# Kernel optimization log

Hardware: AMD Instinct MI355X
Metric: run time of the kernel (lower is better)

Reference implementation:

```python
import jax, jax.numpy as jnp
import numpy as np

B, Q, HIST, HID, NH, D, BS, NBLK, NUMB = 8, 512, 1536, 4096, 32, 128, 64, 32, 256


def _rope(x, pos):
    # GPT-NeoX-style rotary used by Falcon: rotate_half over full head_dim.
    Dh = x.shape[-1]
    inv = 1.0 / (10000.0 ** (jnp.arange(0, Dh, 2, dtype=jnp.float32) / Dh))  # [D/2]
    ang = pos.astype(jnp.float32)[:, None] * inv[None, :]                    # [T, D/2]
    cos = jnp.concatenate([jnp.cos(ang), jnp.cos(ang)], -1)[None, :, None, :]
    sin = jnp.concatenate([jnp.sin(ang), jnp.sin(ang)], -1)[None, :, None, :]
    half = Dh // 2
    rot = jnp.concatenate([-x[..., half:], x[..., :half]], -1)
    return x * cos + rot * sin


def setup_inputs() -> dict:
    key = jax.random.key(0)
    ks = jax.random.split(key, 6)
    hidden_states = jax.random.normal(ks[0], (1, B * Q, HID), jnp.float32) * 0.02
    qkv_weight = jax.random.normal(ks[1], ((NH + 2) * D, HID), jnp.float32) * 0.02
    dense_weight = jax.random.normal(ks[2], (HID, NH * D), jnp.float32) * 0.02
    past_key = jax.random.normal(ks[3], (NUMB, BS, 1, D), jnp.float32) * 0.02
    past_value = jax.random.normal(ks[4], (NUMB, BS, 1, D), jnp.float32) * 0.02
    q_start_loc = (jnp.arange(B) * Q).astype(jnp.int32)
    q_seq_length = jnp.full((B,), Q, jnp.int32)
    history_lengths = jnp.full((B,), HIST, jnp.int32)
    # each sequence owns NBLK distinct cache blocks (shuffled block table)
    block_offsets = jax.random.permutation(ks[5], NUMB).reshape(B, NBLK).astype(jnp.int32)
    position_ids_1d = (history_lengths[:, None] + jnp.arange(Q, dtype=jnp.int32)[None, :]).reshape(-1)
    return dict(hidden_states=hidden_states, qkv_weight=qkv_weight, dense_weight=dense_weight,
                past_key=past_key, past_value=past_value, q_start_loc=q_start_loc,
                q_seq_length=q_seq_length, history_lengths=history_lengths,
                block_offsets=block_offsets, position_ids_1d=position_ids_1d)


def reference(hidden_states, qkv_weight, dense_weight, past_key, past_value,
              q_start_loc, q_seq_length, history_lengths, block_offsets, position_ids_1d):
    T = hidden_states.shape[1]
    Bn = block_offsets.shape[0]
    Qn = T // Bn
    Dh = past_key.shape[-1]
    BSz = past_key.shape[1]
    # fused QKV projection
    fused = hidden_states @ qkv_weight.T                      # [1, T, (NH+2)*D]
    NHh = fused.shape[-1] // Dh - 2
    qkv = fused.reshape(1, T, NHh + 2, Dh)
    q = qkv[:, :, :NHh]                                       # [1, T, NH, D]
    k = qkv[:, :, NHh:NHh + 1]                                 # [1, T, 1, D]
    v = qkv[:, :, NHh + 1:]                                    # [1, T, 1, D]
    # inline rotary embedding on q, k
    q = _rope(q, position_ids_1d)
    k = _rope(k, position_ids_1d)
    # fill_kv_cache: scatter new K/V into paged cache via block table
    seq_id = jnp.repeat(jnp.arange(Bn), Qn)                   # [T]
    pos = position_ids_1d.astype(jnp.int32)                   # absolute kv position
    blk = block_offsets[seq_id, pos // BSz]                   # [T] physical block id
    off = pos % BSz
    past_key = past_key.at[blk, off].set(k.reshape(T, 1, Dh))
    past_value = past_value.at[blk, off].set(v.reshape(T, 1, Dh))
    # paged_attention_fwd: gather per-sequence K/V from paged cache
    KVc = block_offsets.shape[1] * BSz                        # kv capacity == kv_len here
    kseq = past_key[block_offsets].reshape(Bn, KVc, Dh)       # [B, KV, D] (1 kv head squeezed)
    vseq = past_value[block_offsets].reshape(Bn, KVc, Dh)
    qb = q.reshape(Bn, Qn, NHh, Dh)
    scale = 1.0 / jnp.sqrt(jnp.float32(Dh))
    scores = jnp.einsum('bqhd,bkd->bhqk', qb, kseq) * scale   # [B, H, Q, KV]
    qpos = history_lengths[:, None] + jnp.arange(Qn)[None, :] # [B, Q]
    mask = jnp.arange(KVc)[None, None, :] <= qpos[:, :, None] # causal + length mask
    scores = jnp.where(mask[:, None, :, :], scores, jnp.float32(-1e30))
    attn = jax.nn.softmax(scores, axis=-1)
    out = jnp.einsum('bhqk,bkd->bqhd', attn, vseq)            # [B, Q, H, D]
    out = out.reshape(1, T, NHh * Dh)
    return out @ dense_weight.T                                # [1, T, hidden]
```

## Files before the change

### kernel.cpp

```cpp
#include <hip/hip_runtime.h>

typedef __attribute__((ext_vector_type(8))) short bf16x8;
typedef __attribute__((ext_vector_type(4))) float f32x4;
typedef __attribute__((ext_vector_type(16))) float f32x16;
typedef __attribute__((ext_vector_type(2))) unsigned int u32x2;

constexpr int B_ = 8, Q_ = 512, HIST_ = 1536, HID_ = 4096, NH_ = 32, D_ = 128;
constexpr int BS_ = 64, NBLK_ = 32;
constexpr int T_ = B_ * Q_;
constexpr int QKVN = (NH_ + 2) * D_;
constexpr int KVC = NBLK_ * BS_;

__device__ __forceinline__ unsigned short f2bf(float f) {
  union { float f; unsigned u; } v; v.f = f;
  unsigned r = v.u + 0x7FFFu + ((v.u >> 16) & 1u);
  return (unsigned short)(r >> 16);
}
__device__ __forceinline__ float bf2f(unsigned short s) {
  union { unsigned u; float f; } v; v.u = ((unsigned)s) << 16;
  return v.f;
}
__device__ __forceinline__ int cvtpk_bf16(float lo, float hi) {
  int r;
  asm("v_cvt_pk_bf16_f32 %0, %1, %2" : "=v"(r) : "v"(lo), "v"(hi));
  return r;
}

__global__ void k_conv(const float* __restrict__ in, unsigned short* __restrict__ out, int n4) {
  int i = blockIdx.x * blockDim.x + threadIdx.x;
  int stride = gridDim.x * blockDim.x;
  for (; i < n4; i += stride) {
    float4 v = reinterpret_cast<const float4*>(in)[i];
    ushort4 o;
    o.x = f2bf(v.x); o.y = f2bf(v.y); o.z = f2bf(v.z); o.w = f2bf(v.w);
    reinterpret_cast<ushort4*>(out)[i] = o;
  }
}

__global__ void k_gemm_bt(const unsigned short* __restrict__ A,
                          const unsigned short* __restrict__ Bm,
                          float* __restrict__ Cf, unsigned short* __restrict__ Cb,
                          int M, int N, int K, int ldc) {
  __shared__ alignas(16) unsigned short lA[128 * 64];
  __shared__ alignas(16) unsigned short lB[128 * 64];
  const int tid = threadIdx.x;
  const int lane = tid & 63;
  const int w = tid >> 6;
  const int wr = w >> 1, wc = w & 1;
  const int n0 = blockIdx.x * 128, m0 = blockIdx.y * 128;
  const int lr = lane & 15, lk = lane >> 4;
  const int srow = lane >> 3;
  const int scol = (lane & 7) * 8;

  f32x4 acc[4][4];
#pragma unroll
  for (int m = 0; m < 4; ++m)
#pragma unroll
    for (int n = 0; n < 4; ++n) acc[m][n] = f32x4{0.f, 0.f, 0.f, 0.f};

  for (int k0 = 0; k0 < K; k0 += 64) {
#pragma unroll
    for (int i = 0; i < 4; ++i) {
      int seg = w * 4 + i;
      const unsigned short* ga = A + (size_t)(m0 + seg * 8 + srow) * K + k0 + scol;
      const unsigned short* gb = Bm + (size_t)(n0 + seg * 8 + srow) * K + k0 + scol;
      __builtin_amdgcn_global_load_lds((const __attribute__((address_space(1))) void*)ga,
                                       (__attribute__((address_space(3))) void*)(&lA[seg * 512]), 16, 0, 0);
      __builtin_amdgcn_global_load_lds((const __attribute__((address_space(1))) void*)gb,
                                       (__attribute__((address_space(3))) void*)(&lB[seg * 512]), 16, 0, 0);
    }
    __syncthreads();
#pragma unroll
    for (int kk = 0; kk < 2; ++kk) {
      bf16x8 af[4], bfr[4];
      const int sl = (kk * 4 + lk) * 8;
#pragma unroll
      for (int m = 0; m < 4; ++m)
        af[m] = *reinterpret_cast<bf16x8*>(&lA[(wr * 64 + m * 16 + lr) * 64 + sl]);
#pragma unroll
      for (int n = 0; n < 4; ++n)
        bfr[n] = *reinterpret_cast<bf16x8*>(&lB[(wc * 64 + n * 16 + lr) * 64 + sl]);
#pragma unroll
      for (int m = 0; m < 4; ++m)
#pragma unroll
        for (int n = 0; n < 4; ++n)
          acc[m][n] = __builtin_amdgcn_mfma_f32_16x16x32_bf16(af[m], bfr[n], acc[m][n], 0, 0, 0);
    }
    __syncthreads();
  }
#pragma unroll
  for (int m = 0; m < 4; ++m)
#pragma unroll
    for (int n = 0; n < 4; ++n)
#pragma unroll
      for (int j = 0; j < 4; ++j) {
        int r = m0 + wr * 64 + m * 16 + lk * 4 + j;
        int c = n0 + wc * 64 + n * 16 + lr;
        if (Cb) Cb[(size_t)r * ldc + c] = f2bf(acc[m][n][j]);
        else Cf[(size_t)r * ldc + c] = acc[m][n][j];
      }
}

__global__ void k_rope(const unsigned short* __restrict__ fused,
                       const int* __restrict__ pos_ids,
                       unsigned short* __restrict__ qb,
                       unsigned short* __restrict__ kseq,
                       unsigned short* __restrict__ vtg) {
  int t = blockIdx.x;
  int d = threadIdx.x;
  int b = t >> 9, q = t & 511;
  int pos = pos_ids[t];
  __shared__ float cs[64], sn[64];
  if (d < 64) {
    float inv = powf(10000.f, -(float)d * (1.f / 64.f));
    float ang = (float)pos * inv;
    cs[d] = cosf(ang);
    sn[d] = sinf(ang);
  }
  __syncthreads();
  const float scale = 0.1275174313836907f;
  float c = cs[d & 63], s = sn[d & 63];
  const unsigned short* row = fused + (size_t)t * QKVN;
#pragma unroll 4
  for (int h = 0; h < NH_; ++h) {
    float x = bf2f(row[h * D_ + d]);
    float xr = (d < 64) ? -bf2f(row[h * D_ + d + 64]) : bf2f(row[h * D_ + d - 64]);
    qb[(((size_t)(b * NH_ + h)) * Q_ + q) * D_ + d] = f2bf((x * c + xr * s) * scale);
  }
  {
    float x = bf2f(row[NH_ * D_ + d]);
    float xr = (d < 64) ? -bf2f(row[NH_ * D_ + d + 64]) : bf2f(row[NH_ * D_ + d - 64]);
    kseq[((size_t)b * KVC + pos) * D_ + d] = f2bf(x * c + xr * s);
  }
  vtg[((size_t)b * D_ + d) * KVC + pos] = row[(NH_ + 1) * D_ + d];
}

__global__ void k_gather(const float* __restrict__ pk, const float* __restrict__ pv,
                         const int* __restrict__ bo,
                         unsigned short* __restrict__ kseq, unsigned short* __restrict__ vtg) {
  __shared__ unsigned short vl[64 * 140];
  const int ptile = blockIdx.x;
  const int b = ptile / (HIST_ / 64);
  const int p0 = (ptile % (HIST_ / 64)) * 64;
  const int tid = threadIdx.x;
  const int blk = bo[b * NBLK_ + (p0 >> 6)];
#pragma unroll
  for (int c = 0; c < 8; ++c) {
    int u = c * 256 + tid;
    int p = u >> 5, d4 = u & 31;
    size_t src = ((size_t)blk * BS_ + p) * D_ + d4 * 4;
    float4 kv = *reinterpret_cast<const float4*>(pk + src);
    ushort4 ko;
    ko.x = f2bf(kv.x); ko.y = f2bf(kv.y); ko.z = f2bf(kv.z); ko.w = f2bf(kv.w);
    *reinterpret_cast<ushort4*>(kseq + ((size_t)b * KVC + p0 + p) * D_ + d4 * 4) = ko;
    float4 vv = *reinterpret_cast<const float4*>(pv + src);
    ushort4 vo;
    vo.x = f2bf(vv.x); vo.y = f2bf(vv.y); vo.z = f2bf(vv.z); vo.w = f2bf(vv.w);
    *reinterpret_cast<ushort4*>(&vl[p * 140 + d4 * 4]) = vo;
  }
  __syncthreads();
#pragma unroll
  for (int c = 0; c < 4; ++c) {
    int u = c * 256 + tid;
    int d = u >> 3, pg = u & 7;
    bf16x8 vv8;
#pragma unroll
    for (int i = 0; i < 8; ++i) vv8[i] = (short)vl[(pg * 8 + i) * 140 + d];
    *reinterpret_cast<bf16x8*>(vtg + ((size_t)b * D_ + d) * KVC + p0 + pg * 8) = vv8;
  }
}

__global__ __launch_bounds__(512, 2) void k_attn(const unsigned short* __restrict__ qb,
                       const unsigned short* __restrict__ kseq,
                       const unsigned short* __restrict__ vtg,
                       const int* __restrict__ histL,
                       unsigned short* __restrict__ outb) {
  __shared__ alignas(16) unsigned short kl[2][64 * 128];
  __shared__ alignas(16) unsigned short vt[2][128 * 64];
  const int qt = blockIdx.x, hp = blockIdx.y, b = blockIdx.z;
  const int tid = threadIdx.x, lane = tid & 63, w = tid >> 6;
  const int H = lane >> 5, q = lane & 31;
  const int h = hp * 8 + w;
  const int q0 = qt * 32;
  const int hist = histL[b];
  const unsigned short* kseq_b = kseq + (size_t)b * KVC * D_;
  const unsigned short* vtg_b  = vtg + (size_t)b * D_ * KVC;

  const unsigned short* qrow = qb + (((size_t)(b * NH_ + h)) * Q_ + q0 + q) * D_;
  bf16x8 aq[8];
#pragma unroll
  for (int ds = 0; ds < 8; ++ds)
    aq[ds] = *reinterpret_cast<const bf16x8*>(qrow + ds * 16 + H * 8);

  f32x16 o[4];
#pragma unroll
  for (int db = 0; db < 4; ++db)
#pragma unroll
    for (int r = 0; r < 16; ++r) o[db][r] = 0.f;
  float m = -1e30f, l = 0.f;

  const int ntiles = (hist + q0 + 32 + 63) >> 6;

  auto STAGE = [&](int bufi, int kv0) {
#pragma unroll
    for (int c = 0; c < 2; ++c) {
      int ob = c * 8192 + tid * 16;
      int row = ob >> 8;
      int sp = (ob >> 4) & 15;
      const unsigned short* src = kseq_b + (size_t)(kv0 + row) * D_ + (((sp ^ (row & 15)) << 3));
      __builtin_amdgcn_global_load_lds((const __attribute__((address_space(1))) void*)src,
          (__attribute__((address_space(3))) void*)(&kl[bufi][c * 4096 + w * 512]), 16, 0, 0);
    }
#pragma unroll
    for (int c = 0; c < 2; ++c) {
      int ob = c * 8192 + tid * 16;
      int row = ob >> 7;
      int sp = (ob >> 4) & 7;
      const unsigned short* src = vtg_b + (size_t)row * KVC + kv0 + (((sp ^ (row & 7)) << 3));
      __builtin_amdgcn_global_load_lds((const __attribute__((address_space(1))) void*)src,
          (__attribute__((address_space(3))) void*)(&vt[bufi][c * 4096 + w * 512]), 16, 0, 0);
    }
  };

  STAGE(0, 0);
  __syncthreads();

  for (int it = 0; it < ntiles; ++it) {
    const int cur = it & 1;
    if (it + 1 < ntiles) STAGE(cur ^ 1, (it + 1) * 64);
    const unsigned short* kb = kl[cur];
    const unsigned short* vb = vt[cur];

    f32x16 sa = f32x16{0.f,0.f,0.f,0.f,0.f,0.f,0.f,0.f,0.f,0.f,0.f,0.f,0.f,0.f,0.f,0.f};
    f32x16 sb = sa, sc = sa, sd = sa;
#pragma unroll
    for (int ds = 0; ds < 4; ++ds) {
      const int sl = ((2 * ds + H) ^ (q & 15)) << 3;
      bf16x8 k0 = *reinterpret_cast<const bf16x8*>(kb + q * 128 + sl);
      bf16x8 k1 = *reinterpret_cast<const bf16x8*>(kb + (32 + q) * 128 + sl);
      sa = __builtin_amdgcn_mfma_f32_32x32x16_bf16(k0, aq[ds], sa, 0, 0, 0);
      sc = __builtin_amdgcn_mfma_f32_32x32x16_bf16(k1, aq[ds], sc, 0, 0, 0);
    }
#pragma unroll
    for (int ds = 4; ds < 8; ++ds) {
      const int sl = ((2 * ds + H) ^ (q & 15)) << 3;
      bf16x8 k0 = *reinterpret_cast<const bf16x8*>(kb + q * 128 + sl);
      bf16x8 k1 = *reinterpret_cast<const bf16x8*>(kb + (32 + q) * 128 + sl);
      sb = __builtin_amdgcn_mfma_f32_32x32x16_bf16(k0, aq[ds], sb, 0, 0, 0);
      sd = __builtin_amdgcn_mfma_f32_32x32x16_bf16(k1, aq[ds], sd, 0, 0, 0);
    }
    f32x16 s0 = sa + sb;
    f32x16 s1 = sc + sd;

    if (it == ntiles - 1) {
      const int limit = hist + q0 + q - it * 64 - 4 * H;
#pragma unroll
      for (int r = 0; r < 16; ++r) {
        const int koff = (r & 3) + 8 * ((r >> 2) & 1) + 16 * (r >> 3);
        if (koff > limit) s0[r] = -1e30f;
        if (32 + koff > limit) s1[r] = -1e30f;
      }
    }

    float pmax = s0[0];
#pragma unroll
    for (int r = 1; r < 16; ++r) pmax = fmaxf(pmax, s0[r]);
#pragma unroll
    for (int r = 0; r < 16; ++r) pmax = fmaxf(pmax, s1[r]);
    pmax = fmaxf(pmax, __shfl_xor(pmax, 32));
    if (__any(pmax > m + 11.54f)) {
      float mn = fmaxf(m, pmax);
      float al = exp2f(m - mn);
      m = mn;
      l *= al;
#pragma unroll
      for (int db = 0; db < 4; ++db)
#pragma unroll
        for (int r = 0; r < 16; ++r) o[db][r] *= al;
    }
    float rs = 0.f;
#pragma unroll
    for (int r = 0; r < 16; ++r) { s0[r] = exp2f(s0[r] - m); rs += s0[r]; }
#pragma unroll
    for (int r = 0; r < 16; ++r) { s1[r] = exp2f(s1[r] - m); rs += s1[r]; }
    rs += __shfl_xor(rs, 32);
    l += rs;

#pragma unroll
    for (int s = 0; s < 4; ++s) {
      float p0, p1, p2, p3, p4, p5, p6, p7;
      if (s == 0)      { p0=s0[0];p1=s0[1];p2=s0[2];p3=s0[3];p4=s0[4];p5=s0[5];p6=s0[6];p7=s0[7]; }
      else if (s == 1) { p0=s0[8];p1=s0[9];p2=s0[10];p3=s0[11];p4=s0[12];p5=s0[13];p6=s0[14];p7=s0[15]; }
      else if (s == 2) { p0=s1[0];p1=s1[1];p2=s1[2];p3=s1[3];p4=s1[4];p5=s1[5];p6=s1[6];p7=s1[7]; }
      else             { p0=s1[8];p1=s1[9];p2=s1[10];p3=s1[11];p4=s1[12];p5=s1[13];p6=s1[14];p7=s1[15]; }
      int c01 = cvtpk_bf16(p0, p1);
      int c23 = cvtpk_bf16(p2, p3);
      int c45 = cvtpk_bf16(p4, p5);
      int c67 = cvtpk_bf16(p6, p7);
      u32x2 rA = __builtin_amdgcn_permlane32_swap(c01, c45, false, false);
      u32x2 rB = __builtin_amdgcn_permlane32_swap(c23, c67, false, false);
      union { unsigned wds[4]; bf16x8 v; } uu;
      uu.wds[0] = rA[0]; uu.wds[1] = rB[0]; uu.wds[2] = rA[1]; uu.wds[3] = rB[1];
#pragma unroll
      for (int db = 0; db < 4; ++db) {
        const int row = db * 32 + q;
        bf16x8 vf = *reinterpret_cast<const bf16x8*>(vb + row * 64 + ((((2 * s + H) ^ (row & 7))) << 3));
        o[db] = __builtin_amdgcn_mfma_f32_32x32x16_bf16(vf, uu.v, o[db], 0, 0, 0);
      }
    }
    __syncthreads();
  }

  const float il = 1.f / l;
  unsigned short* orow = outb + (size_t)(b * Q_ + q0 + q) * (NH_ * D_) + h * D_;
#pragma unroll
  for (int db = 0; db < 4; ++db)
#pragma unroll
    for (int rr = 0; rr < 4; ++rr) {
      ushort4 st;
      st.x = f2bf(o[db][rr * 4 + 0] * il);
      st.y = f2bf(o[db][rr * 4 + 1] * il);
      st.z = f2bf(o[db][rr * 4 + 2] * il);
      st.w = f2bf(o[db][rr * 4 + 3] * il);
      *reinterpret_cast<ushort4*>(orow + db * 32 + rr * 8 + 4 * H) = st;
    }
}

extern "C" void kernel_launch(void* const* d_in, const int* in_sizes, int n_in,
                              void* d_out, int out_size, void* d_ws, size_t ws_size,
                              hipStream_t stream) {
  const float* hidden = (const float*)d_in[0];
  const float* qkvw   = (const float*)d_in[1];
  const float* densew = (const float*)d_in[2];
  const float* pk     = (const float*)d_in[3];
  const float* pv     = (const float*)d_in[4];
  const int* histL    = (const int*)d_in[7];
  const int* bo       = (const int*)d_in[8];
  const int* posids   = (const int*)d_in[9];
  float* out = (float*)d_out;

  char* ws = (char*)d_ws;
  unsigned short* ws_hidden = (unsigned short*)(ws);
  unsigned short* ws_w      = (unsigned short*)(ws + 33554432);
  unsigned short* ws_fused  = (unsigned short*)(ws + 69206016);
  unsigned short* ws_q      = (unsigned short*)(ws + 104857600);
  unsigned short* ws_k      = (unsigned short*)(ws + 138412032);
  unsigned short* ws_vt     = (unsigned short*)(ws + 142606336);
  unsigned short* ws_attn   = ws_hidden;

  k_conv<<<2048, 256, 0, stream>>>(hidden, ws_hidden, T_ * HID_ / 4);
  k_conv<<<2048, 256, 0, stream>>>(qkvw, ws_w, QKVN * HID_ / 4);
  dim3 g1(QKVN / 128, T_ / 128);
  k_gemm_bt<<<g1, 256, 0, stream>>>(ws_hidden, ws_w, nullptr, ws_fused, T_, QKVN, HID_, QKVN);
  k_rope<<<T_, 128, 0, stream>>>(ws_fused, posids, ws_q, ws_k, ws_vt);
  k_gather<<<B_ * (HIST_ / 64), 256, 0, stream>>>(pk, pv, bo, ws_k, ws_vt);
  dim3 ga(Q_ / 32, NH_ / 8, B_);
  k_attn<<<ga, 512, 0, stream>>>(ws_q, ws_k, ws_vt, histL, ws_attn);
  k_conv<<<2048, 256, 0, stream>>>(densew, ws_w, HID_ * HID_ / 4);
  dim3 g2(HID_ / 128, T_ / 128);
  k_gemm_bt<<<g2, 256, 0, stream>>>(ws_attn, ws_w, out, nullptr, T_, HID_, HID_, HID_);
}
```

Baseline: 600.8 us.

## Replace GEMM with 256x256 double-buffered, swizzled, XCD-remapped pipelined kernel

```diff
diff --git a/kernel.cpp b/kernel.cpp
--- a/kernel.cpp
+++ b/kernel.cpp
@@ -37,67 +37,109 @@
   }
 }
 
-__global__ void k_gemm_bt(const unsigned short* __restrict__ A,
+__global__ __launch_bounds__(512, 2) void k_gemm256(const unsigned short* __restrict__ A,
                           const unsigned short* __restrict__ Bm,
                           float* __restrict__ Cf, unsigned short* __restrict__ Cb,
-                          int M, int N, int K, int ldc) {
-  __shared__ alignas(16) unsigned short lA[128 * 64];
-  __shared__ alignas(16) unsigned short lB[128 * 64];
-  const int tid = threadIdx.x;
-  const int lane = tid & 63;
-  const int w = tid >> 6;
-  const int wr = w >> 1, wc = w & 1;
-  const int n0 = blockIdx.x * 128, m0 = blockIdx.y * 128;
+                          int MB, int K, int ldc) {
+  extern __shared__ unsigned short smem[];
+  unsigned short* sA = smem;
+  unsigned short* sB = smem + 32768;
+  const int tid = threadIdx.x, lane = tid & 63, w = tid >> 6;
+  const int wr = w >> 2, wc = w & 3;
   const int lr = lane & 15, lk = lane >> 4;
-  const int srow = lane >> 3;
-  const int scol = (lane & 7) * 8;
-
-  f32x4 acc[4][4];
-#pragma unroll
-  for (int m = 0; m < 4; ++m)
-#pragma unroll
-    for (int n = 0; n < 4; ++n) acc[m][n] = f32x4{0.f, 0.f, 0.f, 0.f};
-
-  for (int k0 = 0; k0 < K; k0 += 64) {
-#pragma unroll
-    for (int i = 0; i < 4; ++i) {
-      int seg = w * 4 + i;
-      const unsigned short* ga = A + (size_t)(m0 + seg * 8 + srow) * K + k0 + scol;
-      const unsigned short* gb = Bm + (size_t)(n0 + seg * 8 + srow) * K + k0 + scol;
-      __builtin_amdgcn_global_load_lds((const __attribute__((address_space(1))) void*)ga,
-                                       (__attribute__((address_space(3))) void*)(&lA[seg * 512]), 16, 0, 0);
-      __builtin_amdgcn_global_load_lds((const __attribute__((address_space(1))) void*)gb,
-                                       (__attribute__((address_space(3))) void*)(&lB[seg * 512]), 16, 0, 0);
-    }
-    __syncthreads();
-#pragma unroll
-    for (int kk = 0; kk < 2; ++kk) {
-      bf16x8 af[4], bfr[4];
-      const int sl = (kk * 4 + lk) * 8;
-#pragma unroll
-      for (int m = 0; m < 4; ++m)
-        af[m] = *reinterpret_cast<bf16x8*>(&lA[(wr * 64 + m * 16 + lr) * 64 + sl]);
-#pragma unroll
-      for (int n = 0; n < 4; ++n)
-        bfr[n] = *reinterpret_cast<bf16x8*>(&lB[(wc * 64 + n * 16 + lr) * 64 + sl]);
-#pragma unroll
-      for (int m = 0; m < 4; ++m)
+
+  const int nwg = gridDim.x, orig = blockIdx.x;
+  const int q8 = nwg >> 3, r8 = nwg & 7, xcd = orig & 7;
+  const int wg = (xcd < r8 ? xcd * (q8 + 1) : r8 * (q8 + 1) + (xcd - r8) * q8) + (orig >> 3);
+  const int m0 = (wg % MB) * 256;
+  const int n0 = (wg / MB) * 256;
+  const int NT = K >> 6;
+
+  f32x4 acc[8][4];
+#pragma unroll
+  for (int mf = 0; mf < 8; ++mf)
+#pragma unroll
+    for (int nf = 0; nf < 4; ++nf) acc[mf][nf] = f32x4{0.f, 0.f, 0.f, 0.f};
+
+  auto stage = [&](const unsigned short* __restrict__ Mat, int rbase, unsigned short* regionBase,
+                   int ts, int half) {
+    const int di = ts < NT ? ts : NT - 1;
+    const size_t k0 = (size_t)di << 6;
+    char* hb = (char*)(regionBase + (ts & 1) * 16384 + half * 8192);
+#pragma unroll
+    for (int c = 0; c < 2; ++c) {
+      const int ob = c * 8192 + (w << 10) + (lane << 4);
+      const int row = ob >> 7;
+      const int sl = ((ob >> 4) & 7) ^ (row & 7);
+      const unsigned short* src = Mat + (size_t)(rbase + half * 128 + row) * K + k0 + sl * 8;
+      __builtin_amdgcn_global_load_lds((const __attribute__((address_space(1))) void*)src,
+          (__attribute__((address_space(3))) void*)(hb + c * 8192 + (w << 10)), 16, 0, 0);
+    }
+  };
+
+  stage(A, m0, sA, 0, 0); stage(A, m0, sA, 0, 1);
+  stage(Bm, n0, sB, 0, 0); stage(Bm, n0, sB, 0, 1);
+  stage(Bm, n0, sB, 1, 0); stage(Bm, n0, sB, 1, 1);
+  asm volatile("s_waitcnt vmcnt(4)" ::: "memory");
+  __builtin_amdgcn_s_barrier();
+
+  for (int t = 0; t < NT; ++t) {
+    const int cur = t & 1;
+    unsigned short* a_t = sA + cur * 16384 + wr * 8192;
+    unsigned short* b_t = sB + cur * 16384 + (wc >> 1) * 8192;
+    bf16x8 bfr[4][2];
+#pragma unroll
+    for (int p = 0; p < 4; ++p) {
+      bf16x8 af[2][2];
+#pragma unroll
+      for (int m = 0; m < 2; ++m)
+#pragma unroll
+        for (int kk = 0; kk < 2; ++kk) {
+          const int r = p * 32 + m * 16 + lr;
+          af[m][kk] = *reinterpret_cast<bf16x8*>(&a_t[r * 64 + ((((kk << 2) + lk) ^ (r & 7)) << 3)]);
+        }
+      if (p == 0) {
 #pragma unroll
         for (int n = 0; n < 4; ++n)
-          acc[m][n] = __builtin_amdgcn_mfma_f32_16x16x32_bf16(af[m], bfr[n], acc[m][n], 0, 0, 0);
-    }
-    __syncthreads();
-  }
-#pragma unroll
-  for (int m = 0; m < 4; ++m)
-#pragma unroll
-    for (int n = 0; n < 4; ++n)
+#pragma unroll
+          for (int kk = 0; kk < 2; ++kk) {
+            const int rb = (wc & 1) * 64 + n * 16 + lr;
+            bfr[n][kk] = *reinterpret_cast<bf16x8*>(&b_t[rb * 64 + ((((kk << 2) + lk) ^ (rb & 7)) << 3)]);
+          }
+      }
+      if (p == 0) stage(A, m0, sA, t + 1, 0);
+      if (p == 1) { stage(A, m0, sA, t + 1, 1); stage(Bm, n0, sB, t + 2, 0); }
+      if (p == 2) stage(Bm, n0, sB, t + 2, 1);
+      asm volatile("" ::: "memory");
+      __builtin_amdgcn_s_barrier();
+      asm volatile("s_waitcnt lgkmcnt(0)" ::: "memory");
+      __builtin_amdgcn_sched_barrier(0);
+      __builtin_amdgcn_s_setprio(1);
+#pragma unroll
+      for (int m = 0; m < 2; ++m)
+#pragma unroll
+        for (int n = 0; n < 4; ++n)
+#pragma unroll
+          for (int kk = 0; kk < 2; ++kk)
+            acc[p * 2 + m][n] = __builtin_amdgcn_mfma_f32_16x16x32_bf16(af[m][kk], bfr[n][kk], acc[p * 2 + m][n], 0, 0, 0);
+      __builtin_amdgcn_s_setprio(0);
+      if (p == 3) asm volatile("s_waitcnt vmcnt(4)" ::: "memory");
+      asm volatile("" ::: "memory");
+      __builtin_amdgcn_s_barrier();
+    }
+  }
+  asm volatile("s_waitcnt vmcnt(0)" ::: "memory");
+
+#pragma unroll
+  for (int mf = 0; mf < 8; ++mf)
+#pragma unroll
+    for (int nf = 0; nf < 4; ++nf)
 #pragma unroll
       for (int j = 0; j < 4; ++j) {
-        int r = m0 + wr * 64 + m * 16 + lk * 4 + j;
-        int c = n0 + wc * 64 + n * 16 + lr;
-        if (Cb) Cb[(size_t)r * ldc + c] = f2bf(acc[m][n][j]);
-        else Cf[(size_t)r * ldc + c] = acc[m][n][j];
+        const int rr = m0 + wr * 128 + mf * 16 + lk * 4 + j;
+        const int cc = n0 + wc * 64 + nf * 16 + lr;
+        if (Cb) Cb[(size_t)rr * ldc + cc] = f2bf(acc[mf][nf][j]);
+        else Cf[(size_t)rr * ldc + cc] = acc[mf][nf][j];
       }
 }
 
@@ -350,13 +392,13 @@
 
   k_conv<<<2048, 256, 0, stream>>>(hidden, ws_hidden, T_ * HID_ / 4);
   k_conv<<<2048, 256, 0, stream>>>(qkvw, ws_w, QKVN * HID_ / 4);
-  dim3 g1(QKVN / 128, T_ / 128);
-  k_gemm_bt<<<g1, 256, 0, stream>>>(ws_hidden, ws_w, nullptr, ws_fused, T_, QKVN, HID_, QKVN);
+  k_gemm256<<<dim3((T_ / 256) * (QKVN / 256)), 512, 131072, stream>>>(
+      ws_hidden, ws_w, nullptr, ws_fused, T_ / 256, HID_, QKVN);
   k_rope<<<T_, 128, 0, stream>>>(ws_fused, posids, ws_q, ws_k, ws_vt);
   k_gather<<<B_ * (HIST_ / 64), 256, 0, stream>>>(pk, pv, bo, ws_k, ws_vt);
   dim3 ga(Q_ / 32, NH_ / 8, B_);
   k_attn<<<ga, 512, 0, stream>>>(ws_q, ws_k, ws_vt, histL, ws_attn);
   k_conv<<<2048, 256, 0, stream>>>(densew, ws_w, HID_ * HID_ / 4);
-  dim3 g2(HID_ / 128, T_ / 128);
-  k_gemm_bt<<<g2, 256, 0, stream>>>(ws_attn, ws_w, out, nullptr, T_, HID_, HID_, HID_);
-}
+  k_gemm256<<<dim3((T_ / 256) * (HID_ / 256)), 512, 131072, stream>>>(
+      ws_attn, ws_w, out, nullptr, T_ / 256, HID_, HID_);
+}
```

New measurement: 580.7 us. 1.03x faster.

## Rewrite GEMM with 128x256 tiles, triple-buffered LDS pipeline and swizzle

Applied to the files above, without the earlier changes.

```diff
diff --git a/kernel.cpp b/kernel.cpp
--- a/kernel.cpp
+++ b/kernel.cpp
@@ -37,20 +37,25 @@
   }
 }
 
-__global__ void k_gemm_bt(const unsigned short* __restrict__ A,
+#define SW_(r) ((((r) & 3)) ^ (((r) >> 2) & 3))
+
+__global__ __launch_bounds__(512, 4) void k_gemm(const unsigned short* __restrict__ A,
                           const unsigned short* __restrict__ Bm,
                           float* __restrict__ Cf, unsigned short* __restrict__ Cb,
-                          int M, int N, int K, int ldc) {
-  __shared__ alignas(16) unsigned short lA[128 * 64];
-  __shared__ alignas(16) unsigned short lB[128 * 64];
-  const int tid = threadIdx.x;
-  const int lane = tid & 63;
-  const int w = tid >> 6;
-  const int wr = w >> 1, wc = w & 1;
-  const int n0 = blockIdx.x * 128, m0 = blockIdx.y * 128;
+                          int MB, int K, int ldc) {
+  extern __shared__ unsigned short smem[];
+  unsigned short* sA = smem;
+  unsigned short* sB = smem + 12288;
+  const int tid = threadIdx.x, lane = tid & 63, w = tid >> 6;
+  const int wr = w >> 2, wc = w & 3;
   const int lr = lane & 15, lk = lane >> 4;
-  const int srow = lane >> 3;
-  const int scol = (lane & 7) * 8;
+
+  const int nwg = gridDim.x, orig = blockIdx.x;
+  const int q8 = nwg >> 3, r8 = nwg & 7, xcd = orig & 7;
+  const int wg = (xcd < r8 ? xcd * (q8 + 1) : r8 * (q8 + 1) + (xcd - r8) * q8) + (orig >> 3);
+  const int m0 = (wg % MB) * 128;
+  const int n0 = (wg / MB) * 256;
+  const int NT = K >> 5;
 
   f32x4 acc[4][4];
 #pragma unroll
@@ -58,46 +63,77 @@
 #pragma unroll
     for (int n = 0; n < 4; ++n) acc[m][n] = f32x4{0.f, 0.f, 0.f, 0.f};
 
-  for (int k0 = 0; k0 < K; k0 += 64) {
-#pragma unroll
-    for (int i = 0; i < 4; ++i) {
-      int seg = w * 4 + i;
-      const unsigned short* ga = A + (size_t)(m0 + seg * 8 + srow) * K + k0 + scol;
-      const unsigned short* gb = Bm + (size_t)(n0 + seg * 8 + srow) * K + k0 + scol;
-      __builtin_amdgcn_global_load_lds((const __attribute__((address_space(1))) void*)ga,
-                                       (__attribute__((address_space(3))) void*)(&lA[seg * 512]), 16, 0, 0);
-      __builtin_amdgcn_global_load_lds((const __attribute__((address_space(1))) void*)gb,
-                                       (__attribute__((address_space(3))) void*)(&lB[seg * 512]), 16, 0, 0);
-    }
-    __syncthreads();
-#pragma unroll
-    for (int kk = 0; kk < 2; ++kk) {
-      bf16x8 af[4], bfr[4];
-      const int sl = (kk * 4 + lk) * 8;
-#pragma unroll
-      for (int m = 0; m < 4; ++m)
-        af[m] = *reinterpret_cast<bf16x8*>(&lA[(wr * 64 + m * 16 + lr) * 64 + sl]);
+  auto stage = [&](int bi, int k0) {
+    {
+      const int ob = tid << 4;
+      const int row = ob >> 6;
+      const int s = (ob >> 4) & 3;
+      const unsigned short* src = A + (size_t)(m0 + row) * K + k0 + ((s ^ SW_(row)) << 3);
+      __builtin_amdgcn_global_load_lds((const __attribute__((address_space(1))) void*)src,
+          (__attribute__((address_space(3))) void*)((char*)sA + bi * 8192 + (tid << 4)), 16, 0, 0);
+    }
+#pragma unroll
+    for (int c = 0; c < 2; ++c) {
+      const int u = (c << 9) + tid;
+      const int ob = u << 4;
+      const int row = ob >> 6;
+      const int s = (ob >> 4) & 3;
+      const unsigned short* src = Bm + (size_t)(n0 + row) * K + k0 + ((s ^ SW_(row)) << 3);
+      __builtin_amdgcn_global_load_lds((const __attribute__((address_space(1))) void*)src,
+          (__attribute__((address_space(3))) void*)((char*)sB + bi * 16384 + (ob)), 16, 0, 0);
+    }
+  };
+
+  stage(0, 0);
+  stage(1, NT > 1 ? 32 : 0);
+  asm volatile("s_waitcnt vmcnt(3)" ::: "memory");
+  __builtin_amdgcn_s_barrier();
+  asm volatile("" ::: "memory");
+
+  int cur = 0;
+  for (int t = 0; t < NT; ++t) {
+    int sb = cur + 2; if (sb > 2) sb -= 3;
+    const int ts = (t + 2 < NT) ? (t + 2) : (NT - 1);
+    stage(sb, ts << 5);
+
+    const unsigned short* a_t = sA + cur * 4096;
+    const unsigned short* b_t = sB + cur * 8192;
+    bf16x8 af[4], bfr[4];
+#pragma unroll
+    for (int m = 0; m < 4; ++m) {
+      const int r = wr * 64 + m * 16 + lr;
+      af[m] = *reinterpret_cast<const bf16x8*>(&a_t[r * 32 + ((lk ^ SW_(r)) << 3)]);
+    }
+#pragma unroll
+    for (int n = 0; n < 4; ++n) {
+      const int r = wc * 64 + n * 16 + lr;
+      bfr[n] = *reinterpret_cast<const bf16x8*>(&b_t[r * 32 + ((lk ^ SW_(r)) << 3)]);
+    }
+    __builtin_amdgcn_s_setprio(1);
+#pragma unroll
+    for (int m = 0; m < 4; ++m)
 #pragma unroll
       for (int n = 0; n < 4; ++n)
-        bfr[n] = *reinterpret_cast<bf16x8*>(&lB[(wc * 64 + n * 16 + lr) * 64 + sl]);
-#pragma unroll
-      for (int m = 0; m < 4; ++m)
-#pragma unroll
-        for (int n = 0; n < 4; ++n)
-          acc[m][n] = __builtin_amdgcn_mfma_f32_16x16x32_bf16(af[m], bfr[n], acc[m][n], 0, 0, 0);
-    }
-    __syncthreads();
-  }
+        acc[m][n] = __builtin_amdgcn_mfma_f32_16x16x32_bf16(af[m], bfr[n], acc[m][n], 0, 0, 0);
+    __builtin_amdgcn_s_setprio(0);
+
+    asm volatile("s_waitcnt vmcnt(3)" ::: "memory");
+    __builtin_amdgcn_s_barrier();
+    asm volatile("" ::: "memory");
+    cur = (cur == 2) ? 0 : cur + 1;
+  }
+  asm volatile("s_waitcnt vmcnt(0)" ::: "memory");
+
 #pragma unroll
   for (int m = 0; m < 4; ++m)
 #pragma unroll
     for (int n = 0; n < 4; ++n)
 #pragma unroll
       for (int j = 0; j < 4; ++j) {
-        int r = m0 + wr * 64 + m * 16 + lk * 4 + j;
-        int c = n0 + wc * 64 + n * 16 + lr;
-        if (Cb) Cb[(size_t)r * ldc + c] = f2bf(acc[m][n][j]);
-        else Cf[(size_t)r * ldc + c] = acc[m][n][j];
+        const int rr = m0 + wr * 64 + m * 16 + lk * 4 + j;
+        const int cc = n0 + wc * 64 + n * 16 + lr;
+        if (Cb) Cb[(size_t)rr * ldc + cc] = f2bf(acc[m][n][j]);
+        else Cf[(size_t)rr * ldc + cc] = acc[m][n][j];
       }
 }
 
@@ -350,13 +386,13 @@
 
   k_conv<<<2048, 256, 0, stream>>>(hidden, ws_hidden, T_ * HID_ / 4);
   k_conv<<<2048, 256, 0, stream>>>(qkvw, ws_w, QKVN * HID_ / 4);
-  dim3 g1(QKVN / 128, T_ / 128);
-  k_gemm_bt<<<g1, 256, 0, stream>>>(ws_hidden, ws_w, nullptr, ws_fused, T_, QKVN, HID_, QKVN);
+  k_gemm<<<dim3((T_ / 128) * (QKVN / 256)), 512, 73728, stream>>>(
+      ws_hidden, ws_w, nullptr, ws_fused, T_ / 128, HID_, QKVN);
   k_rope<<<T_, 128, 0, stream>>>(ws_fused, posids, ws_q, ws_k, ws_vt);
   k_gather<<<B_ * (HIST_ / 64), 256, 0, stream>>>(pk, pv, bo, ws_k, ws_vt);
   dim3 ga(Q_ / 32, NH_ / 8, B_);
   k_attn<<<ga, 512, 0, stream>>>(ws_q, ws_k, ws_vt, histL, ws_attn);
   k_conv<<<2048, 256, 0, stream>>>(densew, ws_w, HID_ * HID_ / 4);
-  dim3 g2(HID_ / 128, T_ / 128);
-  k_gemm_bt<<<g2, 256, 0, stream>>>(ws_attn, ws_w, out, nullptr, T_, HID_, HID_, HID_);
-}
+  k_gemm<<<dim3((T_ / 128) * (HID_ / 256)), 512, 73728, stream>>>(
+      ws_attn, ws_w, out, nullptr, T_ / 128, HID_, HID_);
+}
```

After: 574.5 us. 1.05x faster.
